# Performance work log

Measured on AMD Instinct MI355X. Metric: run time of the kernel, lower is better.

Reference implementation:

```python
import jax, jax.numpy as jnp
import numpy as np

# Config mirrors Voxelization(__init__) with training=True -> max_voxels[0]
VOXEL_SIZE = (0.05, 0.05, 0.1)
PC_LO = (0.0, -40.0, -3.0)
PC_HI = (70.4, 40.0, 1.0)
MAX_POINTS = 64
MAX_VOXELS = 60000
GX = int(round((PC_HI[0] - PC_LO[0]) / VOXEL_SIZE[0]))  # 1408
GY = int(round((PC_HI[1] - PC_LO[1]) / VOXEL_SIZE[1]))  # 1600
GZ = int(round((PC_HI[2] - PC_LO[2]) / VOXEL_SIZE[2]))  # 40
SENT = GX * GY * GZ  # sentinel linear id for out-of-range points


def setup_inputs() -> dict:
    key = jax.random.key(0)
    u = jax.random.uniform(key, (2_000_000, 4), dtype=jnp.float32)
    lo = jnp.array([PC_LO[0], PC_LO[1], PC_LO[2], 0.0], jnp.float32)
    span = jnp.array([PC_HI[0] - PC_LO[0], PC_HI[1] - PC_LO[1], PC_HI[2] - PC_LO[2], 1.0], jnp.float32)
    points = lo + u * span  # xyz inside range, intensity in [0,1)
    return {"points": points}


def _voxelize(points):
    N, C = points.shape
    vs = jnp.array(VOXEL_SIZE, jnp.float32)
    lo = jnp.array(PC_LO, jnp.float32)
    grid = jnp.array([GX, GY, GZ], jnp.int32)

    g = jnp.floor((points[:, :3] - lo) / vs).astype(jnp.int32)  # [N,3] grid coords (x,y,z)
    valid = jnp.all((g >= 0) & (g < grid), axis=1)
    lin = (g[:, 0] * GY + g[:, 1]) * GZ + g[:, 2]
    lin = jnp.where(valid, lin, SENT).astype(jnp.int32)

    # Stable sort by voxel id; ties keep original point order (deterministic mode)
    order = jnp.argsort(lin)  # jnp.argsort is stable
    sl = lin[order]
    idx = jnp.arange(N, dtype=jnp.int32)
    is_start = jnp.concatenate([jnp.ones((1,), bool), sl[1:] != sl[:-1]])
    gid_sorted = (jnp.cumsum(is_start) - 1).astype(jnp.int32)  # sorted-group id per sorted point

    # First original point index per group -> first-occurrence voxel ordering
    group_first = jnp.full((N,), N, jnp.int32).at[gid_sorted].min(
        jnp.where(is_start, order.astype(jnp.int32), N))
    group_lin = jnp.full((N,), SENT, jnp.int32).at[gid_sorted].min(sl)
    group_first = jnp.where(group_lin == SENT, N, group_first)  # sentinel group ranks last
    perm = jnp.argsort(group_first)  # rank -> group
    inv_rank = jnp.zeros((N,), jnp.int32).at[perm].set(idx)  # group -> rank

    num_valid = jnp.sum(is_start & (sl != SENT)).astype(jnp.int32)
    voxel_num = jnp.minimum(num_valid, MAX_VOXELS)

    # Position within voxel (point order within group)
    start_idx = jax.lax.cummax(jnp.where(is_start, idx, -1))
    pos_sorted = idx - start_idx

    gid = jnp.zeros((N,), jnp.int32).at[order].set(gid_sorted)
    pos = jnp.zeros((N,), jnp.int32).at[order].set(pos_sorted)
    rank = inv_rank[gid]
    keep = valid & (rank < MAX_VOXELS) & (pos < MAX_POINTS)
    rk = jnp.where(keep, rank, MAX_VOXELS)  # OOB -> dropped
    pk = jnp.where(keep, pos, MAX_POINTS)

    voxels = jnp.zeros((MAX_VOXELS, MAX_POINTS, C), points.dtype).at[rk, pk].set(points, mode='drop')
    coors = jnp.zeros((MAX_VOXELS, 3), jnp.int32).at[rk].set(g[:, ::-1], mode='drop')  # flip -> (z,y,x)
    group_count = jnp.zeros((N,), jnp.int32).at[gid_sorted].add((sl != SENT).astype(jnp.int32))
    npv = jnp.minimum(group_count[perm], MAX_POINTS)[:MAX_VOXELS].astype(jnp.int32)
    return voxels, coors, npv, voxel_num


def reference(points):
    # Padded equivalent of torch output (voxels[:n], coors[:n].flip(-1), npv[:n]):
    # rows >= voxel_num are zero; voxel_num gives the true count.
    return _voxelize(points)
```

## Files before the change

kernel.cpp:

```cpp
#include <hip/hip_runtime.h>


#define MAXV 60000
#define MAXP 64
#define FCUT 131072
#define NBUCK 256
#define BSHIFT 14
#define BSLOTS 16384
#define TMASK (NBUCK * BSLOTS - 1)
#define BCAP 10240
#define ECAP 1024
#define BIN_CHUNK 4096
#define SCAN_T 1024
#define CHUNK 2048

typedef unsigned long long u64;

__device__ __forceinline__ int compute_lin(float x, float y, float z) {
  float fx = floorf((x - 0.0f) / 0.05f);
  float fy = floorf((y - (-40.0f)) / 0.05f);
  float fz = floorf((z - (-3.0f)) / 0.1f);
  if (!(fx >= 0.0f && fx < 1408.0f &&
        fy >= 0.0f && fy < 1600.0f &&
        fz >= 0.0f && fz < 40.0f))
    return -1;
  return (((int)fx) * 1600 + (int)fy) * 40 + (int)fz;
}

__device__ __forceinline__ unsigned hash_s(int lin) {
  unsigned h = (unsigned)lin * 2654435761u;
  return (h ^ (h >> 15)) & TMASK;
}

__global__ __launch_bounds__(256) void k_binA(const float4* __restrict__ pts,
                                              int N, u64* __restrict__ binned,
                                              int* __restrict__ bucketCnt) {
  __shared__ int hist[NBUCK];
  __shared__ int lbase[NBUCK];
  __shared__ int cursor[NBUCK];
  __shared__ int gbase[NBUCK];
  __shared__ int totSh;
  __shared__ u64 stage[BIN_CHUNK];

  int tid = threadIdx.x;
  int blockStart = blockIdx.x * BIN_CHUNK;
  hist[tid] = 0;
  __syncthreads();

  unsigned sArr[16];
  int linArr[16];
#pragma unroll
  for (int j = 0; j < 16; j++) {
    int i = blockStart + j * 256 + tid;
    unsigned sv = 0xFFFFFFFFu; int lv = 0;
    if (i < N) {
      float4 p = pts[i];
      int lin = compute_lin(p.x, p.y, p.z);
      if (lin >= 0) {
        sv = hash_s(lin);
        lv = lin;
        atomicAdd(&hist[sv >> BSHIFT], 1);
      }
    }
    sArr[j] = sv; linArr[j] = lv;
  }
  __syncthreads();

  int v = hist[tid];
  lbase[tid] = v;
  __syncthreads();
  for (int off = 1; off < 256; off <<= 1) {
    int t = (tid >= off) ? lbase[tid - off] : 0;
    __syncthreads();
    lbase[tid] += t;
    __syncthreads();
  }
  int excl = lbase[tid] - v;
  __syncthreads();
  lbase[tid] = excl;
  cursor[tid] = excl;
  __syncthreads();

#pragma unroll
  for (int j = 0; j < 16; j++) {
    if (sArr[j] != 0xFFFFFFFFu) {
      int b = (int)(sArr[j] >> BSHIFT);
      int k = atomicAdd(&cursor[b], 1);
      int i = blockStart + j * 256 + tid;
      stage[k] = ((u64)(unsigned)linArr[j] << 32) | (unsigned)i;
    }
  }
  __syncthreads();

  int cntB = cursor[tid] - lbase[tid];
  if (cntB > 0) gbase[tid] = atomicAdd(&bucketCnt[tid], cntB);
  if (tid == 255) totSh = cursor[255];
  __syncthreads();

  int tot = totSh;
  for (int k = tid; k < tot; k += 256) {
    u64 e = stage[k];
    int b = (int)(hash_s((int)(e >> 32)) >> BSHIFT);
    int off = gbase[b] + (k - lbase[b]);
    if (off < BCAP) binned[(size_t)b * BCAP + off] = e;
  }
}

__global__ __launch_bounds__(1024) void k_binB(
    const u64* __restrict__ binned, const int* __restrict__ bucketCnt,
    u64* __restrict__ fs, u64* __restrict__ gEbuf, int* __restrict__ bcnt,
    int* __restrict__ occPartials) {
  __shared__ u64 tab[BSLOTS];
  __shared__ u64 ev[ECAP];
  __shared__ int evCnt;
  __shared__ int occTot;

  int tid = threadIdx.x;
  int b = blockIdx.x;
  for (int k = tid; k < BSLOTS; k += 1024) tab[k] = ~0ull;
  if (tid == 0) { evCnt = 0; occTot = 0; }
  __syncthreads();

  int n = bucketCnt[b]; if (n > BCAP) n = BCAP;
  for (int k = tid; k < n; k += 1024) {
    u64 e = binned[(size_t)b * BCAP + k];
    int i = (int)(unsigned)e;
    int lin = (int)(e >> 32);
    int ls = (int)(hash_s(lin) & (BSLOTS - 1));
    u64 mine = ((u64)(unsigned)i << 40) | ((u64)(unsigned)lin << 12);
    for (;;) {
      u64 cur = tab[ls];
      if (cur == ~0ull) {
        u64 prev = atomicCAS(&tab[ls], ~0ull, mine);
        if (prev == ~0ull) break;
        cur = prev;
      }
      if (((cur >> 12) & 0xFFFFFFFull) == (u64)(unsigned)lin) {
        for (;;) {
          unsigned f = (unsigned)(cur >> 40);
          unsigned c = (unsigned)(cur & 0xFFFu);
          unsigned nf = ((unsigned)i < f) ? (unsigned)i : f;
          unsigned rec = ((unsigned)i < f) ? f : (unsigned)i;
          unsigned nc = (c < 0xFFFu) ? c + 1 : 0xFFFu;
          u64 nv = ((u64)nf << 40) | ((u64)(unsigned)lin << 12) | nc;
          u64 prev = atomicCAS(&tab[ls], cur, nv);
          if (prev == cur) {
            unsigned pos = c + 1;
            if (pos < MAXP) {
              int eidx = atomicAdd(&evCnt, 1);
              if (eidx < ECAP)
                ev[eidx] = ((u64)ls << 40) | ((u64)pos << 24) | rec;
            }
            break;
          }
          cur = prev;
        }
        break;
      }
      ls = (ls + 1) & (BSLOTS - 1);
    }
  }
  __syncthreads();

  int ec = evCnt; if (ec > ECAP) ec = ECAP;
  for (int k = tid; k < ec; k += 1024) {
    u64 e = ev[k];
    int ls = (int)(e >> 40);
    u64 pm = (e >> 24) & 0xFFFFull;
    unsigned rec = (unsigned)(e & 0xFFFFFFu);
    unsigned f = (unsigned)(tab[ls] >> 40);
    gEbuf[(size_t)b * ECAP + k] =
        (f < FCUT) ? (((u64)f << 40) | (pm << 24) | rec) : ~0ull;
  }
  if (tid == 0) bcnt[b] = ec;

  int occ = 0;
  for (int k = tid; k < BSLOTS; k += 1024) {
    u64 w = tab[k];
    if (w != ~0ull) {
      occ++;
      unsigned f = (unsigned)(w >> 40);
      if (f < FCUT) {
        unsigned lin = (unsigned)((w >> 12) & 0xFFFFFFFull);
        unsigned c = (unsigned)(w & 0xFFFu) + 1;
        if (c > MAXP) c = MAXP;
        fs[f] = ((u64)lin << 8) | c;
      }
    }
  }
  for (int off = 32; off > 0; off >>= 1) occ += __shfl_down(occ, off);
  if ((tid & 63) == 0) atomicAdd(&occTot, occ);
  __syncthreads();
  if (tid == 0) occPartials[b] = occTot;
}

__global__ void k_flag_reduce(const u64* __restrict__ fs, int M,
                              int* __restrict__ partials) {
  int tid = threadIdx.x;
  int base = blockIdx.x * CHUNK + tid * 8;
  int sum = 0;
#pragma unroll
  for (int j = 0; j < 8; j++) {
    int i = base + j;
    if (i < M && (long long)fs[i] >= 0) sum++;
  }
  __shared__ int sd[256];
  sd[tid] = sum;
  __syncthreads();
  for (int off = 128; off > 0; off >>= 1) {
    if (tid < off) sd[tid] += sd[tid + off];
    __syncthreads();
  }
  if (tid == 0) partials[blockIdx.x] = sd[0];
}

__global__ void k_scan_partials(int* __restrict__ partials, int NB,
                                const int* __restrict__ occPartials, int nOcc,
                                float* __restrict__ outNum) {
  __shared__ int sd[SCAN_T];
  __shared__ int Dsh;
  int tid = threadIdx.x;

  int acc = 0;
  for (int i = tid; i < nOcc; i += SCAN_T) acc += occPartials[i];
  sd[tid] = acc;
  __syncthreads();
  for (int off = SCAN_T / 2; off > 0; off >>= 1) {
    if (tid < off) sd[tid] += sd[tid + off];
    __syncthreads();
  }
  if (tid == 0) Dsh = sd[0];
  __syncthreads();

  int i0 = 2 * tid, i1 = 2 * tid + 1;
  int a = (i0 < NB) ? partials[i0] : 0;
  int b = (i1 < NB) ? partials[i1] : 0;
  int s = a + b;
  sd[tid] = s;
  __syncthreads();
  for (int off = 1; off < SCAN_T; off <<= 1) {
    int v = (tid >= off) ? sd[tid - off] : 0;
    __syncthreads();
    sd[tid] += v;
    __syncthreads();
  }
  int incl = sd[tid];
  int exclPair = incl - s;
  if (i0 < NB) partials[i0] = exclPair;
  if (i1 < NB) partials[i1] = exclPair + a;
  if (tid == SCAN_T - 1) {
    int D = Dsh;
    outNum[0] = (float)(D < MAXV ? D : MAXV);
  }
}

__global__ void k_rank(const u64* __restrict__ fs,
                       const int* __restrict__ partials,
                       const float4* __restrict__ pts,
                       int* __restrict__ rankOf,
                       float* __restrict__ outCoors, float* __restrict__ outNpv,
                       float4* __restrict__ outVox, int M) {
  int tid = threadIdx.x;
  int base = blockIdx.x * CHUNK + tid * 8;
  u64 v[8];
  int sum = 0;
#pragma unroll
  for (int j = 0; j < 8; j++) {
    int i = base + j;
    v[j] = (i < M) ? fs[i] : ~0ull;
    sum += ((long long)v[j] >= 0) ? 1 : 0;
  }
  __shared__ int sd[256];
  sd[tid] = sum;
  __syncthreads();
  for (int off = 1; off < 256; off <<= 1) {
    int t = (tid >= off) ? sd[tid - off] : 0;
    __syncthreads();
    sd[tid] += t;
    __syncthreads();
  }
  int run = partials[blockIdx.x] + sd[tid] - sum;
#pragma unroll
  for (int j = 0; j < 8; j++) {
    if ((long long)v[j] >= 0) {
      int f = base + j;
      int r = run++;
      rankOf[f] = r;
      if (r < MAXV) {
        int lin = (int)(v[j] >> 8);
        int gz = lin % 40;
        int t = lin / 40;
        int gy = t % 1600;
        int gx = t / 1600;
        outCoors[r * 3 + 0] = (float)gz;
        outCoors[r * 3 + 1] = (float)gy;
        outCoors[r * 3 + 2] = (float)gx;
        outNpv[r] = (float)(int)(v[j] & 0xFF);
        outVox[(size_t)r * MAXP] = pts[f];
      }
    }
  }
}

__global__ void k_events(const float4* __restrict__ pts,
                         const int* __restrict__ bcnt,
                         const u64* __restrict__ gEbuf,
                         const int* __restrict__ rankOf,
                         float4* __restrict__ outVox) {
  int gid = blockIdx.x * 256 + threadIdx.x;
  int b = gid >> 10;
  int t = gid & (ECAP - 1);
  if (t >= bcnt[b]) return;
  u64 e = gEbuf[(size_t)b * ECAP + t];
  if (e == ~0ull) return;
  unsigned f = (unsigned)(e >> 40);
  unsigned pos = (unsigned)((e >> 24) & 0xFFFFu);
  unsigned rec = (unsigned)(e & 0xFFFFFFu);
  int r = rankOf[f];
  if ((unsigned)r >= (unsigned)MAXV) return;
  outVox[(size_t)r * MAXP + pos] = pts[rec];
}

extern "C" void kernel_launch(void* const* d_in, const int* in_sizes, int n_in,
                              void* d_out, int out_size, void* d_ws, size_t ws_size,
                              hipStream_t stream) {
  const float4* pts = (const float4*)d_in[0];
  int N = in_sizes[0] / 4;

  float* out = (float*)d_out;
  float* outVox = out;
  float* outCoors = out + (size_t)MAXV * MAXP * 4;
  float* outNpv = outCoors + (size_t)MAXV * 3;
  float* outNum = outNpv + MAXV;

  char* w = (char*)d_ws;
  u64* binned = (u64*)w;         w += (size_t)NBUCK * BCAP * 8;
  u64* gEbuf = (u64*)w;          w += (size_t)NBUCK * ECAP * 8;
  int* rankOf = (int*)w;         w += (size_t)FCUT * 4;
  int* partials = (int*)w;       w += 1024;
  int* occPartials = (int*)w;    w += NBUCK * 4;
  int* bcnt = (int*)w;           w += NBUCK * 4;
  u64* fs = (u64*)w;             w += (size_t)FCUT * 8;
  int* bucketCnt = (int*)w;      w += NBUCK * 4;

  hipMemsetAsync(d_out, 0, (size_t)out_size * sizeof(float), stream);
  hipMemsetAsync(fs, 0xFF, (size_t)FCUT * 8, stream);
  hipMemsetAsync(bucketCnt, 0, NBUCK * 4, stream);

  int nbA = (N + BIN_CHUNK - 1) / BIN_CHUNK;
  int NB = FCUT / CHUNK;

  k_binA<<<nbA, 256, 0, stream>>>(pts, N, binned, bucketCnt);
  k_binB<<<NBUCK, 1024, 0, stream>>>(binned, bucketCnt, fs, gEbuf, bcnt,
                                     occPartials);
  k_flag_reduce<<<NB, 256, 0, stream>>>(fs, FCUT, partials);
  k_scan_partials<<<1, SCAN_T, 0, stream>>>(partials, NB, occPartials, NBUCK,
                                            outNum);
  k_rank<<<NB, 256, 0, stream>>>(fs, partials, pts, rankOf,
                                 outCoors, outNpv, (float4*)outVox, FCUT);
  k_events<<<NBUCK * ECAP / 256, 256, 0, stream>>>(pts, bcnt, gEbuf, rankOf,
                                                   (float4*)outVox);
}
```

Before: 158.4 us.

## Replace full output memset with in-kernel row zeroing and merge workspace memsets

Drops the large memset of the whole voxel output. Instead, k_rank zero-fills each written voxel row after storing its first point, and k_events zero-fills rows from the voxel count up to MAXV, which now comes through a new workspace int. The fs empty sentinel changes from all-ones to zero so fs and bucketCnt can be cleared with one contiguous memset. Also vectorises the shared hash-table init and scan, and does the insertion CAS directly without a prior load. This aims to cut the redundant double write of the ~61MB output, at the risk of poorly coalesced per-thread row stores and correctness relying on every rank below the count being produced by k_rank.

```diff
diff --git a/kernel.cpp b/kernel.cpp
--- a/kernel.cpp
+++ b/kernel.cpp
@@ -117,7 +117,8 @@
 
   int tid = threadIdx.x;
   int b = blockIdx.x;
-  for (int k = tid; k < BSLOTS; k += 1024) tab[k] = ~0ull;
+  for (int k = tid; k < BSLOTS / 2; k += 1024)
+    ((ulonglong2*)tab)[k] = make_ulonglong2(~0ull, ~0ull);
   if (tid == 0) { evCnt = 0; occTot = 0; }
   __syncthreads();
 
@@ -129,12 +130,8 @@
     int ls = (int)(hash_s(lin) & (BSLOTS - 1));
     u64 mine = ((u64)(unsigned)i << 40) | ((u64)(unsigned)lin << 12);
     for (;;) {
-      u64 cur = tab[ls];
-      if (cur == ~0ull) {
-        u64 prev = atomicCAS(&tab[ls], ~0ull, mine);
-        if (prev == ~0ull) break;
-        cur = prev;
-      }
+      u64 cur = atomicCAS(&tab[ls], ~0ull, mine);
+      if (cur == ~0ull) break;
       if (((cur >> 12) & 0xFFFFFFFull) == (u64)(unsigned)lin) {
         for (;;) {
           unsigned f = (unsigned)(cur >> 40);
@@ -175,16 +172,20 @@
   if (tid == 0) bcnt[b] = ec;
 
   int occ = 0;
-  for (int k = tid; k < BSLOTS; k += 1024) {
-    u64 w = tab[k];
-    if (w != ~0ull) {
-      occ++;
-      unsigned f = (unsigned)(w >> 40);
-      if (f < FCUT) {
-        unsigned lin = (unsigned)((w >> 12) & 0xFFFFFFFull);
-        unsigned c = (unsigned)(w & 0xFFFu) + 1;
-        if (c > MAXP) c = MAXP;
-        fs[f] = ((u64)lin << 8) | c;
+  for (int k = tid; k < BSLOTS / 2; k += 1024) {
+    ulonglong2 w2 = ((const ulonglong2*)tab)[k];
+#pragma unroll
+    for (int h = 0; h < 2; h++) {
+      u64 w = h ? w2.y : w2.x;
+      if (w != ~0ull) {
+        occ++;
+        unsigned f = (unsigned)(w >> 40);
+        if (f < FCUT) {
+          unsigned lin = (unsigned)((w >> 12) & 0xFFFFFFFull);
+          unsigned c = (unsigned)(w & 0xFFFu) + 1;
+          if (c > MAXP) c = MAXP;
+          fs[f] = ((u64)lin << 8) | c;
+        }
       }
     }
   }
@@ -202,7 +203,7 @@
 #pragma unroll
   for (int j = 0; j < 8; j++) {
     int i = base + j;
-    if (i < M && (long long)fs[i] >= 0) sum++;
+    if (i < M && fs[i] != 0) sum++;
   }
   __shared__ int sd[256];
   sd[tid] = sum;
@@ -216,7 +217,8 @@
 
 __global__ void k_scan_partials(int* __restrict__ partials, int NB,
                                 const int* __restrict__ occPartials, int nOcc,
-                                float* __restrict__ outNum) {
+                                float* __restrict__ outNum,
+                                int* __restrict__ Dws) {
   __shared__ int sd[SCAN_T];
   __shared__ int Dsh;
   int tid = threadIdx.x;
@@ -250,7 +252,9 @@
   if (i1 < NB) partials[i1] = exclPair + a;
   if (tid == SCAN_T - 1) {
     int D = Dsh;
-    outNum[0] = (float)(D < MAXV ? D : MAXV);
+    int vn = D < MAXV ? D : MAXV;
+    outNum[0] = (float)vn;
+    Dws[0] = vn;
   }
 }
 
@@ -267,8 +271,8 @@
 #pragma unroll
   for (int j = 0; j < 8; j++) {
     int i = base + j;
-    v[j] = (i < M) ? fs[i] : ~0ull;
-    sum += ((long long)v[j] >= 0) ? 1 : 0;
+    v[j] = (i < M) ? fs[i] : 0;
+    sum += (v[j] != 0) ? 1 : 0;
   }
   __shared__ int sd[256];
   sd[tid] = sum;
@@ -282,7 +286,7 @@
   int run = partials[blockIdx.x] + sd[tid] - sum;
 #pragma unroll
   for (int j = 0; j < 8; j++) {
-    if ((long long)v[j] >= 0) {
+    if (v[j] != 0) {
       int f = base + j;
       int r = run++;
       rankOf[f] = r;
@@ -296,7 +300,11 @@
         outCoors[r * 3 + 1] = (float)gy;
         outCoors[r * 3 + 2] = (float)gx;
         outNpv[r] = (float)(int)(v[j] & 0xFF);
-        outVox[(size_t)r * MAXP] = pts[f];
+        float4* row = outVox + (size_t)r * MAXP;
+        row[0] = pts[f];
+        float4 z = make_float4(0.f, 0.f, 0.f, 0.f);
+#pragma unroll
+        for (int q = 1; q < MAXP; q++) row[q] = z;
       }
     }
   }
@@ -306,8 +314,21 @@
                          const int* __restrict__ bcnt,
                          const u64* __restrict__ gEbuf,
                          const int* __restrict__ rankOf,
+                         const int* __restrict__ Dws,
+                         float* __restrict__ outCoors,
+                         float* __restrict__ outNpv,
                          float4* __restrict__ outVox) {
   int gid = blockIdx.x * 256 + threadIdx.x;
+
+  int D = Dws[0];
+  for (int r = D + gid; r < MAXV; r += NBUCK * ECAP) {
+    float4* row = outVox + (size_t)r * MAXP;
+    float4 z = make_float4(0.f, 0.f, 0.f, 0.f);
+    for (int q = 0; q < MAXP; q++) row[q] = z;
+    outCoors[r * 3 + 0] = 0.f; outCoors[r * 3 + 1] = 0.f;
+    outCoors[r * 3 + 2] = 0.f; outNpv[r] = 0.f;
+  }
+
   int b = gid >> 10;
   int t = gid & (ECAP - 1);
   if (t >= bcnt[b]) return;
@@ -340,12 +361,13 @@
   int* partials = (int*)w;       w += 1024;
   int* occPartials = (int*)w;    w += NBUCK * 4;
   int* bcnt = (int*)w;           w += NBUCK * 4;
+  int* Dws = (int*)w;            w += 256;
+  char* z0 = w;
   u64* fs = (u64*)w;             w += (size_t)FCUT * 8;
   int* bucketCnt = (int*)w;      w += NBUCK * 4;
-
-  hipMemsetAsync(d_out, 0, (size_t)out_size * sizeof(float), stream);
-  hipMemsetAsync(fs, 0xFF, (size_t)FCUT * 8, stream);
-  hipMemsetAsync(bucketCnt, 0, NBUCK * 4, stream);
+  size_t zBytes = (size_t)(w - z0);
+
+  hipMemsetAsync(z0, 0, zBytes, stream);
 
   int nbA = (N + BIN_CHUNK - 1) / BIN_CHUNK;
   int NB = FCUT / CHUNK;
@@ -355,9 +377,10 @@
                                      occPartials);
   k_flag_reduce<<<NB, 256, 0, stream>>>(fs, FCUT, partials);
   k_scan_partials<<<1, SCAN_T, 0, stream>>>(partials, NB, occPartials, NBUCK,
-                                            outNum);
+                                            outNum, Dws);
   k_rank<<<NB, 256, 0, stream>>>(fs, partials, pts, rankOf,
                                  outCoors, outNpv, (float4*)outVox, FCUT);
   k_events<<<NBUCK * ECAP / 256, 256, 0, stream>>>(pts, bcnt, gEbuf, rankOf,
+                                                   Dws, outCoors, outNpv,
                                                    (float4*)outVox);
 }
```

Result: slower. 214.6 us (+35.5%).
